# Performance work log

Hardware: AMD Instinct MI355X
Metric: run time of the kernel (lower is better)

## Reference

```python
import jax, jax.numpy as jnp
import numpy as np

N_EMBD = 1024
N_HEAD = 16
BLOCK_SIZE = 2048


def setup_inputs() -> dict:
    key = jax.random.key(0)
    k1, k2, k3 = jax.random.split(key, 3)
    B, T, C = 2, 2048, N_EMBD
    x = jax.random.normal(k1, (B, T, C), dtype=jnp.float32)
    # Dense(3*n_embd, use_bias=False): kernel [C, 3C]
    Wqkv = jax.random.normal(k2, (C, 3 * C), dtype=jnp.float32) * (1.0 / np.sqrt(C))
    # Output Dense(n_embd): kernel [C, C] + bias [C]
    Wout = jax.random.normal(k3, (C, C), dtype=jnp.float32) * (1.0 / np.sqrt(C))
    bout = jnp.zeros((C,), dtype=jnp.float32)
    return {"x": x, "Wqkv": Wqkv, "Wout": Wout, "bout": bout}


def reference(x, Wqkv, Wout, bout):
    B, T, C = x.shape
    H = N_HEAD
    hs = C // H  # head_size

    qkv = x @ Wqkv                       # [B, T, 3C]
    q, k, v = jnp.split(qkv, 3, axis=-1)  # each [B, T, C]
    q = q.reshape(B, T, H, hs).transpose(0, 2, 1, 3)  # [B, H, T, hs]
    k = k.reshape(B, T, H, hs).transpose(0, 2, 1, 3)
    v = v.reshape(B, T, H, hs).transpose(0, 2, 1, 3)

    att = jnp.einsum("bhqd,bhkd->bhqk", q, k) * (hs ** -0.5)  # [B, H, T, T]
    T_use = min(T, BLOCK_SIZE)
    mask = jnp.tril(jnp.ones((T_use, T_use), dtype=bool))
    att = jnp.where(mask, att, -jnp.inf)
    att = jax.nn.softmax(att, axis=-1)
    # dropout: deterministic (training=False) -> identity

    out = jnp.einsum("bhqk,bhkd->bhqd", att, v)  # [B, H, T, hs]
    out = out.transpose(0, 2, 1, 3).reshape(B, T, C)
    out = out @ Wout + bout
    return out
```

## Files before the change

kernel.cpp:

```cpp
#include <hip/hip_runtime.h>
#include <cstdint>
#include <cstddef>

#define BB 2
#define TT 2048
#define CC 1024
#define HH 16
#define HS 64
#define MM (BB*TT)
#define N1 (3*CC)

#define PST2 40

#define QSCALE 0.1803368801111243f

typedef __bf16 bf16_t;
typedef bf16_t bf16x8 __attribute__((ext_vector_type(8)));
typedef float  floatx4 __attribute__((ext_vector_type(4)));

__device__ __forceinline__ bf16_t f2bf(float f) {
    uint32_t u = __builtin_bit_cast(uint32_t, f);
    u += 0x7FFFu + ((u >> 16) & 1u);
    unsigned short s = (unsigned short)(u >> 16);
    return __builtin_bit_cast(bf16_t, s);
}

__device__ __forceinline__ void load_lds16(const bf16_t* g, bf16_t* l) {
    __builtin_amdgcn_global_load_lds((__attribute__((address_space(1))) void*)g,
                                     (__attribute__((address_space(3))) void*)l,
                                     16, 0, 0);
}

__device__ __forceinline__ void transpose_body(const float* __restrict__ src,
                                               bf16_t* __restrict__ dst,
                                               int R, int Ccol, int bx, int by,
                                               int tx, int ty, bf16_t (*tile)[33]) {
    int c0 = bx * 32, r0 = by * 32;
    for (int i = ty; i < 32; i += 8)
        tile[i][tx] = f2bf(src[(size_t)(r0 + i) * Ccol + c0 + tx]);
    __syncthreads();
    for (int i = ty; i < 32; i += 8)
        dst[(size_t)(c0 + i) * R + r0 + tx] = tile[tx][i];
}

__global__ __launch_bounds__(256) void k_prep(const float* __restrict__ x,
                                              const float* __restrict__ Wqkv,
                                              const float* __restrict__ Wout,
                                              bf16_t* __restrict__ xb,
                                              bf16_t* __restrict__ Wt1,
                                              bf16_t* __restrict__ Wt2) {
    __shared__ bf16_t tile[32][33];
    const int bid = blockIdx.x, tid = threadIdx.x;
    if (bid < 2048) {
        size_t i = ((size_t)bid * 256 + tid) * 8;
        float4 a = *(const float4*)(x + i);
        float4 b = *(const float4*)(x + i + 4);
        bf16x8 o;
        o[0] = f2bf(a.x); o[1] = f2bf(a.y); o[2] = f2bf(a.z); o[3] = f2bf(a.w);
        o[4] = f2bf(b.x); o[5] = f2bf(b.y); o[6] = f2bf(b.z); o[7] = f2bf(b.w);
        *(bf16x8*)(xb + i) = o;
    } else if (bid < 2048 + 3072) {
        int bb = bid - 2048;
        transpose_body(Wqkv, Wt1, CC, N1, bb % 96, bb / 96, tid & 31, tid >> 5, tile);
    } else {
        int bb = bid - 5120;
        transpose_body(Wout, Wt2, CC, CC, bb & 31, bb >> 5, tid & 31, tid >> 5, tile);
    }
}

__device__ __forceinline__ void gemm_core(const bf16_t* __restrict__ A,
                                          const bf16_t* __restrict__ Bt,
                                          bf16_t* As, bf16_t* Bs,
                                          int m0, int n0, int K,
                                          floatx4 acc[4][4]) {
    const int tid = threadIdx.x;
    const int wave = tid >> 6, lane = tid & 63;
    const int quad = lane >> 4, lrow = lane & 15;
    const int wm = wave >> 1, wn = wave & 1;
    const int lsub = lane >> 2;
    const int kc = lane & 3;

    for (int kk = 0; kk < K; kk += 32) {
        for (int s = 0; s < 2; ++s) {
            int rg = wave * 2 + s;
            const bf16_t* ga = A  + (size_t)(m0 + rg * 16 + lsub) * K + kk + kc * 8;
            const bf16_t* gb = Bt + (size_t)(n0 + rg * 16 + lsub) * K + kk + kc * 8;
            load_lds16(ga, As + rg * 512);
            load_lds16(gb, Bs + rg * 512);
        }
        __syncthreads();
        bf16x8 af[4], bfr[4];
        for (int i = 0; i < 4; ++i)
            af[i] = *(const bf16x8*)(As + (wm * 64 + i * 16 + lrow) * 32 + quad * 8);
        for (int j = 0; j < 4; ++j)
            bfr[j] = *(const bf16x8*)(Bs + (wn * 64 + j * 16 + lrow) * 32 + quad * 8);
        for (int i = 0; i < 4; ++i)
            for (int j = 0; j < 4; ++j)
                acc[i][j] = __builtin_amdgcn_mfma_f32_16x16x32_bf16(af[i], bfr[j], acc[i][j], 0, 0, 0);
        __syncthreads();
    }
}

__global__ __launch_bounds__(512) void k_gemm_qkv(const bf16_t* __restrict__ x,
                                                  const bf16_t* __restrict__ Wt,
                                                  bf16_t* __restrict__ qb,
                                                  bf16_t* __restrict__ kb,
                                                  bf16_t* __restrict__ vt) {
    __shared__ bf16_t As[4][256 * 32];
    __shared__ bf16_t Bs[4][256 * 32];
    const int tid = threadIdx.x;
    const int wave = tid >> 6, lane = tid & 63;
    const int quad = lane >> 4, lrow = lane & 15;
    const int wm = wave >> 2, wn = wave & 3;

    const int bid = blockIdx.y * 12 + blockIdx.x;
    const int swz = (bid & 7) * 24 + (bid >> 3);
    const int m0 = (swz / 12) * 256, n0 = (swz % 12) * 256;

    floatx4 acc[8][4];
    #pragma unroll
    for (int i = 0; i < 8; ++i)
        #pragma unroll
        for (int j = 0; j < 4; ++j) acc[i][j] = floatx4{0.f, 0.f, 0.f, 0.f};

    auto stage = [&](int kt) {
        const int slot = kt & 3;
        const int kk = kt * 32;
        #pragma unroll
        for (int l = 0; l < 2; ++l) {
            int L = l * 512 + tid;
            int row = L >> 2, cs = L & 3;
            int gc = cs ^ ((row >> 1) & 3);
            const bf16_t* ga = x  + (size_t)(m0 + row) * CC + kk + gc * 8;
            const bf16_t* gb = Wt + (size_t)(n0 + row) * CC + kk + gc * 8;
            load_lds16(ga, &As[slot][(size_t)(l * 512 + wave * 64) * 8]);
            load_lds16(gb, &Bs[slot][(size_t)(l * 512 + wave * 64) * 8]);
        }
    };

    auto do_tile = [&](int kt, bool st) {
        const bf16_t* Ab = &As[kt & 3][0];
        const bf16_t* Bb = &Bs[kt & 3][0];
        const int csw = (quad ^ ((lrow >> 1) & 3)) * 8;
        bf16x8 af[8], bfr[4];
        #pragma unroll
        for (int mf = 0; mf < 8; ++mf) {
            int row = wm * 128 + mf * 16 + lrow;
            af[mf] = *(const bf16x8*)(Ab + row * 32 + csw);
        }
        #pragma unroll
        for (int nf = 0; nf < 4; ++nf) {
            int row = wn * 64 + nf * 16 + lrow;
            bfr[nf] = *(const bf16x8*)(Bb + row * 32 + csw);
        }
        if (st) stage(kt + 3);
        __builtin_amdgcn_s_barrier();
        __builtin_amdgcn_s_setprio(1);
        #pragma unroll
        for (int mf = 0; mf < 8; ++mf)
            #pragma unroll
            for (int nf = 0; nf < 4; ++nf)
                acc[mf][nf] = __builtin_amdgcn_mfma_f32_16x16x32_bf16(af[mf], bfr[nf], acc[mf][nf], 0, 0, 0);
        __builtin_amdgcn_s_setprio(0);
    };

    stage(0); stage(1); stage(2);
    asm volatile("s_waitcnt vmcnt(8)" ::: "memory");
    __builtin_amdgcn_s_barrier();

    for (int kt = 0; kt < 29; ++kt) {
        do_tile(kt, true);
        asm volatile("s_waitcnt vmcnt(8)" ::: "memory");
        __builtin_amdgcn_s_barrier();
    }
    do_tile(29, false);
    asm volatile("s_waitcnt vmcnt(4)" ::: "memory");
    __builtin_amdgcn_s_barrier();
    do_tile(30, false);
    asm volatile("s_waitcnt vmcnt(0)" ::: "memory");
    __builtin_amdgcn_s_barrier();
    do_tile(31, false);

    const int b = m0 >> 11;
    #pragma unroll
    for (int nf = 0; nf < 4; ++nf) {
        int gn = n0 + wn * 64 + nf * 16 + lrow;
        int which = gn >> 10, c = gn & 1023, h = c >> 6, d = c & 63;
        if (which == 0) {
            #pragma unroll
            for (int mf = 0; mf < 8; ++mf)
                #pragma unroll
                for (int r = 0; r < 4; ++r) {
                    int t = (m0 & 2047) + wm * 128 + mf * 16 + quad * 4 + r;
                    qb[((size_t)(b * HH + h) * TT + t) * HS + d] = f2bf(acc[mf][nf][r] * QSCALE);
                }
        } else if (which == 1) {
            #pragma unroll
            for (int mf = 0; mf < 8; ++mf)
                #pragma unroll
                for (int r = 0; r < 4; ++r) {
                    int t = (m0 & 2047) + wm * 128 + mf * 16 + quad * 4 + r;
                    kb[((size_t)(b * HH + h) * TT + t) * HS + d] = f2bf(acc[mf][nf][r]);
                }
        } else {
            #pragma unroll
            for (int a = 0; a < 4; ++a) {
                bf16x8 pv;
                #pragma unroll
                for (int r = 0; r < 4; ++r) {
                    pv[r * 2]     = f2bf(acc[2 * a][nf][r]);
                    pv[r * 2 + 1] = f2bf(acc[2 * a + 1][nf][r]);
                }
                int tb2 = (m0 & 2047) + wm * 128 + a * 32;
                *(bf16x8*)(vt + ((size_t)(b * HH + h) * HS + d) * TT + tb2 + quad * 8) = pv;
            }
        }
    }
}

__device__ static const signed char ORD[48][2] = {
    {15,-1},{31,0},{31,1},{30,0},{30,1},
    {14,-1},{29,0},{29,1},{28,0},{28,1},
    {13,-1},{27,0},{27,1},{26,0},{26,1},
    {12,-1},{25,0},{25,1},{24,0},{24,1},
    {11,-1},{23,0},{23,1},{22,0},{22,1},
    {10,-1},{21,0},{21,1},{20,0},{20,1},
    { 9,-1},{19,0},{19,1},{18,0},{18,1},
    { 8,-1},{17,0},{17,1},{16,0},{16,1},
    { 7,-1},{ 6,-1},{ 5,-1},{ 4,-1},{ 3,-1},{ 2,-1},{ 1,-1},{ 0,-1}
};

__global__ __launch_bounds__(128, 2) void k_attn(const bf16_t* __restrict__ qb,
                                                 const bf16_t* __restrict__ kb,
                                                 const bf16_t* __restrict__ vt,
                                                 bf16_t* __restrict__ yb,
                                                 float* __restrict__ o0,
                                                 float* __restrict__ o1,
                                                 float* __restrict__ l0,
                                                 float* __restrict__ l1) {
    __shared__ bf16_t Kb[2][32 * 72];
    __shared__ bf16_t Vb[2][64 * 40];
    __shared__ bf16_t Ps[2][2][32 * PST2];
    const int tid = threadIdx.x;
    const int w = tid >> 6, lane = tid & 63;
    const int quad = lane >> 4, lrow = lane & 15;
    const int bh = blockIdx.x & 31;
    const int j = blockIdx.x >> 5;
    const int qg = ORD[j][0];
    const int cc = ORD[j][1];
    const int ct = (cc < 0) ? (2 * qg + 2) : (qg + 1);
    const int key0 = (cc == 1) ? (qg + 1) * 32 : 0;
    const int kendl = 2 * qg + w + 1 - ((cc == 1) ? (qg + 1) : 0);
    const int kw = min(kendl, ct);
    const int q0 = qg * 64 + w * 32;

    const bf16_t* Qg = qb + (size_t)bh * TT * HS;
    const bf16_t* Kg = kb + (size_t)bh * TT * HS;
    const bf16_t* Vg = vt + (size_t)bh * HS * TT;

    const int skey = tid >> 2, scol = (tid & 3) * 16;
    const int svrow = tid >> 1, svcol = (tid & 1) * 16;

    bf16x8 kra, krb, vra, vrb;
    {
        const bf16_t* gk = Kg + (size_t)(key0 + skey) * HS + scol;
        kra = *(const bf16x8*)(gk);
        krb = *(const bf16x8*)(gk + 8);
        const bf16_t* gv = Vg + (size_t)svrow * TT + key0 + svcol;
        vra = *(const bf16x8*)(gv);
        vrb = *(const bf16x8*)(gv + 8);
        *(bf16x8*)(&Kb[0][skey * 72 + scol])     = kra;
        *(bf16x8*)(&Kb[0][skey * 72 + scol + 8]) = krb;
        *(bf16x8*)(&Vb[0][svrow * 40 + svcol])     = vra;
        *(bf16x8*)(&Vb[0][svrow * 40 + svcol + 8]) = vrb;
    }

    bf16x8 aq[2][2];
    for (int tq = 0; tq < 2; ++tq)
        for (int c = 0; c < 2; ++c)
            aq[tq][c] = *(const bf16x8*)(Qg + (size_t)(q0 + tq * 16 + lrow) * HS + c * 32 + quad * 8);

    const bf16_t onebf = __builtin_bit_cast(bf16_t, (unsigned short)0x3F80);
    bf16x8 bones = {onebf, onebf, onebf, onebf, onebf, onebf, onebf, onebf};

    floatx4 o[2][4];
    for (int tq = 0; tq < 2; ++tq)
        for (int dc = 0; dc < 4; ++dc) o[tq][dc] = floatx4{0.f, 0.f, 0.f, 0.f};
    floatx4 ol[2] = {floatx4{0.f,0.f,0.f,0.f}, floatx4{0.f,0.f,0.f,0.f}};

    bf16x8 bv_sav[4];
    const int wrow0 = quad * 4;

    for (int t = 0; t < ct; ++t) {
        __syncthreads();
        if (t + 1 < ct) {
            const bf16_t* gk = Kg + (size_t)(key0 + (t + 1) * 32 + skey) * HS + scol;
            kra = *(const bf16x8*)(gk);
            krb = *(const bf16x8*)(gk + 8);
            const bf16_t* gv = Vg + (size_t)svrow * TT + key0 + (t + 1) * 32 + svcol;
            vra = *(const bf16x8*)(gv);
            vrb = *(const bf16x8*)(gv + 8);
        }
        if (t < kw) {
            if (t > 0) {
                const bf16_t* Pp = &Ps[w][(t - 1) & 1][0];
                bf16x8 pa0 = *(const bf16x8*)(Pp + (size_t)lrow * PST2 + quad * 8);
                bf16x8 pa1 = *(const bf16x8*)(Pp + (size_t)(16 + lrow) * PST2 + quad * 8);
                o[0][0] = __builtin_amdgcn_mfma_f32_16x16x32_bf16(pa0, bv_sav[0], o[0][0], 0, 0, 0);
                o[0][1] = __builtin_amdgcn_mfma_f32_16x16x32_bf16(pa0, bv_sav[1], o[0][1], 0, 0, 0);
                o[0][2] = __builtin_amdgcn_mfma_f32_16x16x32_bf16(pa0, bv_sav[2], o[0][2], 0, 0, 0);
                o[0][3] = __builtin_amdgcn_mfma_f32_16x16x32_bf16(pa0, bv_sav[3], o[0][3], 0, 0, 0);
                ol[0]   = __builtin_amdgcn_mfma_f32_16x16x32_bf16(pa0, bones, ol[0], 0, 0, 0);
                o[1][0] = __builtin_amdgcn_mfma_f32_16x16x32_bf16(pa1, bv_sav[0], o[1][0], 0, 0, 0);
                o[1][1] = __builtin_amdgcn_mfma_f32_16x16x32_bf16(pa1, bv_sav[1], o[1][1], 0, 0, 0);
                o[1][2] = __builtin_amdgcn_mfma_f32_16x16x32_bf16(pa1, bv_sav[2], o[1][2], 0, 0, 0);
                o[1][3] = __builtin_amdgcn_mfma_f32_16x16x32_bf16(pa1, bv_sav[3], o[1][3], 0, 0, 0);
                ol[1]   = __builtin_amdgcn_mfma_f32_16x16x32_bf16(pa1, bones, ol[1], 0, 0, 0);
            }
            const bf16_t* Kt = &Kb[t & 1][0];
            const bf16_t* Vt = &Vb[t & 1][0];
            bf16x8 bk0 = *(const bf16x8*)(Kt + lrow * 72 + quad * 8);
            bf16x8 bk1 = *(const bf16x8*)(Kt + lrow * 72 + 32 + quad * 8);
            bf16x8 bk2 = *(const bf16x8*)(Kt + (16 + lrow) * 72 + quad * 8);
            bf16x8 bk3 = *(const bf16x8*)(Kt + (16 + lrow) * 72 + 32 + quad * 8);
            floatx4 s00 = floatx4{0.f,0.f,0.f,0.f}, s01 = s00, s10 = s00, s11 = s00;
            s00 = __builtin_amdgcn_mfma_f32_16x16x32_bf16(aq[0][0], bk0, s00, 0, 0, 0);
            s00 = __builtin_amdgcn_mfma_f32_16x16x32_bf16(aq[0][1], bk1, s00, 0, 0, 0);
            s01 = __builtin_amdgcn_mfma_f32_16x16x32_bf16(aq[0][0], bk2, s01, 0, 0, 0);
            s01 = __builtin_amdgcn_mfma_f32_16x16x32_bf16(aq[0][1], bk3, s01, 0, 0, 0);
            s10 = __builtin_amdgcn_mfma_f32_16x16x32_bf16(aq[1][0], bk0, s10, 0, 0, 0);
            s10 = __builtin_amdgcn_mfma_f32_16x16x32_bf16(aq[1][1], bk1, s10, 0, 0, 0);
            s11 = __builtin_amdgcn_mfma_f32_16x16x32_bf16(aq[1][0], bk2, s11, 0, 0, 0);
            s11 = __builtin_amdgcn_mfma_f32_16x16x32_bf16(aq[1][1], bk3, s11, 0, 0, 0);

            bv_sav[0] = *(const bf16x8*)(Vt + (0  + lrow) * 40 + quad * 8);
            bv_sav[1] = *(const bf16x8*)(Vt + (16 + lrow) * 40 + quad * 8);
            bv_sav[2] = *(const bf16x8*)(Vt + (32 + lrow) * 40 + quad * 8);
            bv_sav[3] = *(const bf16x8*)(Vt + (48 + lrow) * 40 + quad * 8);

            uint32_t* P32 = (uint32_t*)(&Ps[w][t & 1][0]);
            if (t < kendl - 1) {
                for (int r = 0; r < 4; ++r) {
                    float e00 = __builtin_amdgcn_exp2f(s00[r]);
                    float e01 = __builtin_amdgcn_exp2f(s01[r]);
                    float e10 = __builtin_amdgcn_exp2f(s10[r]);
                    float e11 = __builtin_amdgcn_exp2f(s11[r]);
                    uint32_t pk0 = __builtin_amdgcn_perm(
                        __builtin_bit_cast(uint32_t, e01),
                        __builtin_bit_cast(uint32_t, e00), 0x07060302u);
                    uint32_t pk1 = __builtin_amdgcn_perm(
                        __builtin_bit_cast(uint32_t, e11),
                        __builtin_bit_cast(uint32_t, e10), 0x07060302u);
                    P32[(wrow0 + r) * 20 + lrow]      = pk0;
                    P32[(wrow0 + r + 16) * 20 + lrow] = pk1;
                }
            } else {
                for (int r = 0; r < 4; ++r) {
                    bool keep = lrow <= quad * 4 + r;
                    float e00 = keep ? __builtin_amdgcn_exp2f(s00[r]) : 0.f;
                    float e01 = 0.f; (void)s01;
                    float e10 = __builtin_amdgcn_exp2f(s10[r]);
                    float e11 = keep ? __builtin_amdgcn_exp2f(s11[r]) : 0.f;
                    uint32_t pk0 = __builtin_amdgcn_perm(
                        __builtin_bit_cast(uint32_t, e01),
                        __builtin_bit_cast(uint32_t, e00), 0x07060302u);
                    uint32_t pk1 = __builtin_amdgcn_perm(
                        __builtin_bit_cast(uint32_t, e11),
                        __builtin_bit_cast(uint32_t, e10), 0x07060302u);
                    P32[(wrow0 + r) * 20 + lrow]      = pk0;
                    P32[(wrow0 + r + 16) * 20 + lrow] = pk1;
                }
            }
        }
        if (t + 1 < ct) {
            bf16_t* Kn = &Kb[(t + 1) & 1][0];
            bf16_t* Vn = &Vb[(t + 1) & 1][0];
            *(bf16x8*)(Kn + skey * 72 + scol)     = kra;
            *(bf16x8*)(Kn + skey * 72 + scol + 8) = krb;
            *(bf16x8*)(Vn + svrow * 40 + svcol)     = vra;
            *(bf16x8*)(Vn + svrow * 40 + svcol + 8) = vrb;
        }
    }

    asm volatile("s_waitcnt lgkmcnt(0)" ::: "memory");
    {
        const bf16_t* Pp = &Ps[w][(kw - 1) & 1][0];
        bf16x8 pa0 = *(const bf16x8*)(Pp + (size_t)lrow * PST2 + quad * 8);
        bf16x8 pa1 = *(const bf16x8*)(Pp + (size_t)(16 + lrow) * PST2 + quad * 8);
        o[0][0] = __builtin_amdgcn_mfma_f32_16x16x32_bf16(pa0, bv_sav[0], o[0][0], 0, 0, 0);
        o[0][1] = __builtin_amdgcn_mfma_f32_16x16x32_bf16(pa0, bv_sav[1], o[0][1], 0, 0, 0);
        o[0][2] = __builtin_amdgcn_mfma_f32_16x16x32_bf16(pa0, bv_sav[2], o[0][2], 0, 0, 0);
        o[0][3] = __builtin_amdgcn_mfma_f32_16x16x32_bf16(pa0, bv_sav[3], o[0][3], 0, 0, 0);
        ol[0]   = __builtin_amdgcn_mfma_f32_16x16x32_bf16(pa0, bones, ol[0], 0, 0, 0);
        o[1][0] = __builtin_amdgcn_mfma_f32_16x16x32_bf16(pa1, bv_sav[0], o[1][0], 0, 0, 0);
        o[1][1] = __builtin_amdgcn_mfma_f32_16x16x32_bf16(pa1, bv_sav[1], o[1][1], 0, 0, 0);
        o[1][2] = __builtin_amdgcn_mfma_f32_16x16x32_bf16(pa1, bv_sav[2], o[1][2], 0, 0, 0);
        o[1][3] = __builtin_amdgcn_mfma_f32_16x16x32_bf16(pa1, bv_sav[3], o[1][3], 0, 0, 0);
        ol[1]   = __builtin_amdgcn_mfma_f32_16x16x32_bf16(pa1, bones, ol[1], 0, 0, 0);
    }

    if (cc < 0) {
        const int b = bh >> 4, h = bh & 15;
        for (int tq = 0; tq < 2; ++tq)
            for (int r = 0; r < 4; ++r) {
                float inv = 1.0f / ol[tq][r];
                int q = q0 + tq * 16 + quad * 4 + r;
                for (int dc = 0; dc < 4; ++dc)
                    yb[(size_t)(b * TT + q) * CC + h * HS + dc * 16 + lrow] =
                        f2bf(o[tq][dc][r] * inv);
            }
    } else if (cc == 1) {
        for (int tq = 0; tq < 2; ++tq)
            for (int r = 0; r < 4; ++r) {
                int q = q0 + tq * 16 + quad * 4 + r;
                float* dst = o1 + ((size_t)(bh * 16 + qg - 16) * 64 + (q - qg * 64)) * 64 + lrow;
                for (int dc = 0; dc < 4; ++dc) dst[dc * 16] = o[tq][dc][r];
                if (lrow == 0) l1[(size_t)(bh * 16 + qg - 16) * 64 + (q - qg * 64)] = ol[tq][r];
            }
    } else {
        for (int tq = 0; tq < 2; ++tq)
            for (int r = 0; r < 4; ++r) {
                int q = q0 + tq * 16 + quad * 4 + r;
                float* dst = o0 + ((size_t)bh * TT + q) * HS + lrow;
                for (int dc = 0; dc < 4; ++dc) dst[dc * 16] = o[tq][dc][r];
                if (lrow == 0) l0[(size_t)bh * TT + q] = ol[tq][r];
            }
    }
}

__global__ __launch_bounds__(256) void k_norm(const float* __restrict__ o0,
                                              const float* __restrict__ o1,
                                              const float* __restrict__ l0,
                                              const float* __restrict__ l1,
                                              bf16_t* __restrict__ yb) {
    int idx = blockIdx.x * 256 + threadIdx.x;
    int d8 = idx & 7;
    int q  = 1024 + ((idx >> 3) & 1023);
    int bh = idx >> 13;
    int qg = q >> 6;
    const float* s0 = o0 + ((size_t)bh * TT + q) * HS + d8 * 8;
    const float* s1 = o1 + ((size_t)(bh * 16 + qg - 16) * 64 + (q & 63)) * 64 + d8 * 8;
    float4 a = *(const float4*)(s0);
    float4 b = *(const float4*)(s0 + 4);
    float4 a1 = *(const float4*)(s1);
    float4 b1 = *(const float4*)(s1 + 4);
    a.x += a1.x; a.y += a1.y; a.z += a1.z; a.w += a1.w;
    b.x += b1.x; b.y += b1.y; b.z += b1.z; b.w += b1.w;
    float l = l0[(size_t)bh * TT + q] + l1[(size_t)(bh * 16 + qg - 16) * 64 + (q & 63)];
    float inv = 1.0f / l;
    bf16x8 r;
    r[0] = f2bf(a.x * inv); r[1] = f2bf(a.y * inv);
    r[2] = f2bf(a.z * inv); r[3] = f2bf(a.w * inv);
    r[4] = f2bf(b.x * inv); r[5] = f2bf(b.y * inv);
    r[6] = f2bf(b.z * inv); r[7] = f2bf(b.w * inv);
    int bb = bh >> 4, h = bh & 15;
    *(bf16x8*)(yb + ((size_t)(bb * TT + q)) * CC + h * HS + d8 * 8) = r;
}

__global__ __launch_bounds__(256, 2) void k_gemm_out(const bf16_t* __restrict__ yin,
                                                     const bf16_t* __restrict__ Wt,
                                                     const float* __restrict__ bias,
                                                     float* __restrict__ out) {
    __shared__ bf16_t As[128 * 32];
    __shared__ bf16_t Bs[128 * 32];
    const int m0 = blockIdx.y * 128, n0 = blockIdx.x * 128;
    floatx4 acc[4][4];
    for (int i = 0; i < 4; ++i)
        for (int j = 0; j < 4; ++j)
            acc[i][j] = floatx4{0.f, 0.f, 0.f, 0.f};
    gemm_core(yin, Wt, As, Bs, m0, n0, CC, acc);

    const int tid = threadIdx.x, wave = tid >> 6, lane = tid & 63;
    const int quad = lane >> 4, lrow = lane & 15;
    const int wm = wave >> 1, wn = wave & 1;
    for (int i = 0; i < 4; ++i)
        for (int j = 0; j < 4; ++j) {
            int gn = n0 + wn * 64 + j * 16 + lrow;
            float bb = bias[gn];
            for (int r = 0; r < 4; ++r) {
                int gm = m0 + wm * 64 + i * 16 + quad * 4 + r;
                out[(size_t)gm * CC + gn] = acc[i][j][r] + bb;
            }
        }
}

extern "C" void kernel_launch(void* const* d_in, const int* in_sizes, int n_in,
                              void* d_out, int out_size, void* d_ws, size_t ws_size,
                              hipStream_t stream) {
    (void)in_sizes; (void)n_in; (void)out_size; (void)ws_size;
    const float* x    = (const float*)d_in[0];
    const float* Wqkv = (const float*)d_in[1];
    const float* Wout = (const float*)d_in[2];
    const float* bout = (const float*)d_in[3];
    float* out = (float*)d_out;

    bf16_t* xb  = (bf16_t*)d_ws;
    bf16_t* Wt1 = xb + (size_t)MM * CC;
    bf16_t* Wt2 = Wt1 + (size_t)N1 * CC;
    bf16_t* qb  = Wt2 + (size_t)CC * CC;
    bf16_t* kb  = qb + (size_t)BB * HH * TT * HS;
    bf16_t* vb  = kb + (size_t)BB * HH * TT * HS;
    bf16_t* yb  = vb + (size_t)BB * HH * TT * HS;
    float*  o0  = (float*)d_out;
    float*  o1  = (float*)xb;
    float*  l0  = (float*)Wt1;
    float*  l1  = l0 + (size_t)BB * HH * TT;

    k_prep<<<dim3(2048 + 3072 + 1024), 256, 0, stream>>>(x, Wqkv, Wout, xb, Wt1, Wt2);
    k_gemm_qkv<<<dim3(N1 / 256, MM / 256), 512, 0, stream>>>(xb, Wt1, qb, kb, vb);
    k_attn<<<dim3(48 * 32), 128, 0, stream>>>(qb, kb, vb, yb, o0, o1, l0, l1);
    k_norm<<<dim3(1024), 256, 0, stream>>>(o0, o1, l0, l1, yb);
    k_gemm_out<<<dim3(CC / 128, MM / 128), 256, 0, stream>>>(yb, Wt2, bout, out);
}
```

Measured before the change: 180.2 us.

## Split QKV GEMM k-tile into two half phases and shrink output GEMM tile

Each k-tile of the QKV GEMM now runs in two halves, each with its own LDS fragment loads, staging of A or B for a later tile, barrier and MFMA batch. This interleaves global-to-LDS prefetch with compute at a finer grain and halves the number of live A fragments. Separately, the output projection GEMM drops from 128x128 to 128x64 tiles, doubling the block count (512 blocks) to fill more CUs. The extra barriers per k-tile add synchronisation cost, and the smaller output tiles give less data reuse per block.

```diff
diff --git a/kernel.cpp b/kernel.cpp
--- a/kernel.cpp
+++ b/kernel.cpp
@@ -68,39 +68,6 @@
     }
 }
 
-__device__ __forceinline__ void gemm_core(const bf16_t* __restrict__ A,
-                                          const bf16_t* __restrict__ Bt,
-                                          bf16_t* As, bf16_t* Bs,
-                                          int m0, int n0, int K,
-                                          floatx4 acc[4][4]) {
-    const int tid = threadIdx.x;
-    const int wave = tid >> 6, lane = tid & 63;
-    const int quad = lane >> 4, lrow = lane & 15;
-    const int wm = wave >> 1, wn = wave & 1;
-    const int lsub = lane >> 2;
-    const int kc = lane & 3;
-
-    for (int kk = 0; kk < K; kk += 32) {
-        for (int s = 0; s < 2; ++s) {
-            int rg = wave * 2 + s;
-            const bf16_t* ga = A  + (size_t)(m0 + rg * 16 + lsub) * K + kk + kc * 8;
-            const bf16_t* gb = Bt + (size_t)(n0 + rg * 16 + lsub) * K + kk + kc * 8;
-            load_lds16(ga, As + rg * 512);
-            load_lds16(gb, Bs + rg * 512);
-        }
-        __syncthreads();
-        bf16x8 af[4], bfr[4];
-        for (int i = 0; i < 4; ++i)
-            af[i] = *(const bf16x8*)(As + (wm * 64 + i * 16 + lrow) * 32 + quad * 8);
-        for (int j = 0; j < 4; ++j)
-            bfr[j] = *(const bf16x8*)(Bs + (wn * 64 + j * 16 + lrow) * 32 + quad * 8);
-        for (int i = 0; i < 4; ++i)
-            for (int j = 0; j < 4; ++j)
-                acc[i][j] = __builtin_amdgcn_mfma_f32_16x16x32_bf16(af[i], bfr[j], acc[i][j], 0, 0, 0);
-        __syncthreads();
-    }
-}
-
 __global__ __launch_bounds__(512) void k_gemm_qkv(const bf16_t* __restrict__ x,
                                                   const bf16_t* __restrict__ Wt,
                                                   bf16_t* __restrict__ qb,
@@ -123,7 +90,7 @@
         #pragma unroll
         for (int j = 0; j < 4; ++j) acc[i][j] = floatx4{0.f, 0.f, 0.f, 0.f};
 
-    auto stage = [&](int kt) {
+    auto stageA = [&](int kt) {
         const int slot = kt & 3;
         const int kk = kt * 32;
         #pragma unroll
@@ -131,55 +98,85 @@
             int L = l * 512 + tid;
             int row = L >> 2, cs = L & 3;
             int gc = cs ^ ((row >> 1) & 3);
-            const bf16_t* ga = x  + (size_t)(m0 + row) * CC + kk + gc * 8;
-            const bf16_t* gb = Wt + (size_t)(n0 + row) * CC + kk + gc * 8;
-            load_lds16(ga, &As[slot][(size_t)(l * 512 + wave * 64) * 8]);
-            load_lds16(gb, &Bs[slot][(size_t)(l * 512 + wave * 64) * 8]);
+            load_lds16(x + (size_t)(m0 + row) * CC + kk + gc * 8,
+                       &As[slot][(size_t)(l * 512 + wave * 64) * 8]);
         }
     };
-
-    auto do_tile = [&](int kt, bool st) {
+    auto stageB = [&](int kt) {
+        const int slot = kt & 3;
+        const int kk = kt * 32;
+        #pragma unroll
+        for (int l = 0; l < 2; ++l) {
+            int L = l * 512 + tid;
+            int row = L >> 2, cs = L & 3;
+            int gc = cs ^ ((row >> 1) & 3);
+            load_lds16(Wt + (size_t)(n0 + row) * CC + kk + gc * 8,
+                       &Bs[slot][(size_t)(l * 512 + wave * 64) * 8]);
+        }
+    };
+
+    const int csw = (quad ^ ((lrow >> 1) & 3)) * 8;
+
+    auto do_ktile = [&](int kt, bool st) {
         const bf16_t* Ab = &As[kt & 3][0];
         const bf16_t* Bb = &Bs[kt & 3][0];
-        const int csw = (quad ^ ((lrow >> 1) & 3)) * 8;
-        bf16x8 af[8], bfr[4];
-        #pragma unroll
-        for (int mf = 0; mf < 8; ++mf) {
-            int row = wm * 128 + mf * 16 + lrow;
-            af[mf] = *(const bf16x8*)(Ab + row * 32 + csw);
-        }
-        #pragma unroll
-        for (int nf = 0; nf < 4; ++nf) {
-            int row = wn * 64 + nf * 16 + lrow;
-            bfr[nf] = *(const bf16x8*)(Bb + row * 32 + csw);
-        }
-        if (st) stage(kt + 3);
-        __builtin_amdgcn_s_barrier();
-        __builtin_amdgcn_s_setprio(1);
-        #pragma unroll
-        for (int mf = 0; mf < 8; ++mf)
+        bf16x8 bfr[4];
+        {
+            bf16x8 af[4];
+            #pragma unroll
+            for (int mf = 0; mf < 4; ++mf)
+                af[mf] = *(const bf16x8*)(Ab + (wm * 128 + mf * 16 + lrow) * 32 + csw);
             #pragma unroll
             for (int nf = 0; nf < 4; ++nf)
-                acc[mf][nf] = __builtin_amdgcn_mfma_f32_16x16x32_bf16(af[mf], bfr[nf], acc[mf][nf], 0, 0, 0);
-        __builtin_amdgcn_s_setprio(0);
+                bfr[nf] = *(const bf16x8*)(Bb + (wn * 64 + nf * 16 + lrow) * 32 + csw);
+            if (st) stageA(kt + 3);
+            __builtin_amdgcn_s_barrier();
+            asm volatile("s_waitcnt lgkmcnt(0)" ::: "memory");
+            __builtin_amdgcn_sched_barrier(0);
+            __builtin_amdgcn_s_setprio(1);
+            #pragma unroll
+            for (int mf = 0; mf < 4; ++mf)
+                #pragma unroll
+                for (int nf = 0; nf < 4; ++nf)
+                    acc[mf][nf] = __builtin_amdgcn_mfma_f32_16x16x32_bf16(af[mf], bfr[nf], acc[mf][nf], 0, 0, 0);
+            __builtin_amdgcn_s_setprio(0);
+            __builtin_amdgcn_s_barrier();
+        }
+        {
+            bf16x8 af[4];
+            #pragma unroll
+            for (int mf = 0; mf < 4; ++mf)
+                af[mf] = *(const bf16x8*)(Ab + (wm * 128 + (mf + 4) * 16 + lrow) * 32 + csw);
+            if (st) stageB(kt + 3);
+            __builtin_amdgcn_s_barrier();
+            asm volatile("s_waitcnt lgkmcnt(0)" ::: "memory");
+            __builtin_amdgcn_sched_barrier(0);
+            __builtin_amdgcn_s_setprio(1);
+            #pragma unroll
+            for (int mf = 0; mf < 4; ++mf)
+                #pragma unroll
+                for (int nf = 0; nf < 4; ++nf)
+                    acc[mf + 4][nf] = __builtin_amdgcn_mfma_f32_16x16x32_bf16(af[mf], bfr[nf], acc[mf + 4][nf], 0, 0, 0);
+            __builtin_amdgcn_s_setprio(0);
+        }
     };
 
-    stage(0); stage(1); stage(2);
+    stageA(0); stageB(0); stageA(1); stageB(1); stageA(2); stageB(2);
     asm volatile("s_waitcnt vmcnt(8)" ::: "memory");
     __builtin_amdgcn_s_barrier();
 
     for (int kt = 0; kt < 29; ++kt) {
-        do_tile(kt, true);
+        do_ktile(kt, true);
         asm volatile("s_waitcnt vmcnt(8)" ::: "memory");
         __builtin_amdgcn_s_barrier();
     }
-    do_tile(29, false);
+    do_ktile(29, false);
     asm volatile("s_waitcnt vmcnt(4)" ::: "memory");
     __builtin_amdgcn_s_barrier();
-    do_tile(30, false);
+    do_ktile(30, false);
     asm volatile("s_waitcnt vmcnt(0)" ::: "memory");
     __builtin_amdgcn_s_barrier();
-    do_tile(31, false);
+    do_ktile(31, false);
 
     const int b = m0 >> 11;
     #pragma unroll
@@ -462,20 +459,42 @@
                                                      const float* __restrict__ bias,
                                                      float* __restrict__ out) {
     __shared__ bf16_t As[128 * 32];
-    __shared__ bf16_t Bs[128 * 32];
-    const int m0 = blockIdx.y * 128, n0 = blockIdx.x * 128;
-    floatx4 acc[4][4];
-    for (int i = 0; i < 4; ++i)
-        for (int j = 0; j < 4; ++j)
-            acc[i][j] = floatx4{0.f, 0.f, 0.f, 0.f};
-    gemm_core(yin, Wt, As, Bs, m0, n0, CC, acc);
-
-    const int tid = threadIdx.x, wave = tid >> 6, lane = tid & 63;
+    __shared__ bf16_t Bs[64 * 32];
+    const int m0 = blockIdx.y * 128, n0 = blockIdx.x * 64;
+    const int tid = threadIdx.x;
+    const int wave = tid >> 6, lane = tid & 63;
     const int quad = lane >> 4, lrow = lane & 15;
     const int wm = wave >> 1, wn = wave & 1;
+    const int lsub = lane >> 2;
+    const int kc = lane & 3;
+
+    floatx4 acc[4][2];
     for (int i = 0; i < 4; ++i)
-        for (int j = 0; j < 4; ++j) {
-            int gn = n0 + wn * 64 + j * 16 + lrow;
+        for (int j = 0; j < 2; ++j) acc[i][j] = floatx4{0.f, 0.f, 0.f, 0.f};
+
+    for (int kk = 0; kk < CC; kk += 32) {
+        for (int s = 0; s < 2; ++s) {
+            int rg = wave * 2 + s;
+            load_lds16(yin + (size_t)(m0 + rg * 16 + lsub) * CC + kk + kc * 8,
+                       As + rg * 512);
+        }
+        load_lds16(Wt + (size_t)(n0 + wave * 16 + lsub) * CC + kk + kc * 8,
+                   Bs + wave * 512);
+        __syncthreads();
+        bf16x8 af[4], bfr[2];
+        for (int i = 0; i < 4; ++i)
+            af[i] = *(const bf16x8*)(As + (wm * 64 + i * 16 + lrow) * 32 + quad * 8);
+        for (int j = 0; j < 2; ++j)
+            bfr[j] = *(const bf16x8*)(Bs + (wn * 32 + j * 16 + lrow) * 32 + quad * 8);
+        for (int i = 0; i < 4; ++i)
+            for (int j = 0; j < 2; ++j)
+                acc[i][j] = __builtin_amdgcn_mfma_f32_16x16x32_bf16(af[i], bfr[j], acc[i][j], 0, 0, 0);
+        __syncthreads();
+    }
+
+    for (int i = 0; i < 4; ++i)
+        for (int j = 0; j < 2; ++j) {
+            int gn = n0 + wn * 32 + j * 16 + lrow;
             float bb = bias[gn];
             for (int r = 0; r < 4; ++r) {
                 int gm = m0 + wm * 64 + i * 16 + quad * 4 + r;
@@ -510,5 +529,5 @@
     k_gemm_qkv<<<dim3(N1 / 256, MM / 256), 512, 0, stream>>>(xb, Wt1, qb, kb, vb);
     k_attn<<<dim3(48 * 32), 128, 0, stream>>>(qb, kb, vb, yb, o0, o1, l0, l1);
     k_norm<<<dim3(1024), 256, 0, stream>>>(o0, o1, l0, l1, yb);
-    k_gemm_out<<<dim3(CC / 128, MM / 128), 256, 0, stream>>>(yb, Wt2, bout, out);
-}
+    k_gemm_out<<<dim3(CC / 64, MM / 128), 256, 0, stream>>>(yb, Wt2, bout, out);
+}
```

New measurement: 182.9 us. No clear change (+1.4%).
